# Kernel optimization log

Measured on AMD Instinct MI355X. Metric: run time of the kernel, lower is better.

The kernel has to match this reference:

```python
import jax, jax.numpy as jnp
import numpy as np

BETA, ALPHA, NS_STEPS = 0.9, 1.0, 1
D_MODEL, D_STATE, D_CONV, EXPAND = 768, 16, 4, 2
D_INNER = EXPAND * D_MODEL
DT_RANK = -(-D_MODEL // 16)  # ceil(d_model/16) = 48
B, L = 2, 1024


def setup_inputs() -> dict:
    key = jax.random.key(0)
    ks = jax.random.split(key, 8)
    s = lambda k, shape, sc=0.02: jax.random.normal(k, shape, jnp.float32) * sc
    return {
        "hidden_states": jax.random.normal(ks[0], (B, L, D_MODEL), jnp.float32),
        "in_proj_w": s(ks[1], (2 * D_INNER, D_MODEL)),
        "conv_w": s(ks[2], (D_INNER, 1, D_CONV), 0.2),
        "conv_b": jnp.zeros((D_INNER,), jnp.float32),
        "x_proj_w": s(ks[3], (DT_RANK + 2 * D_STATE, D_INNER)),
        "dt_head_w": s(ks[4], (D_INNER, DT_RANK)),
        "dt_head_b": s(ks[5], (D_INNER,), 0.1),
        "out_proj_w": s(ks[6], (D_MODEL, D_INNER)),
        "D": jnp.ones((D_INNER,), jnp.float32),
    }


def _newton_schulz(G, steps):
    """Muon-style quintic Newton-Schulz orthogonalization of (b, d, n) with d >= n."""
    a, b, c = 3.4445, -4.7750, 2.0315
    X = G / (jnp.linalg.norm(G, axis=(-2, -1), keepdims=True) + 1e-7)
    X = X.swapaxes(-2, -1)  # (b, n, d): rows <= cols
    for _ in range(steps):
        A = X @ X.swapaxes(-2, -1)       # (b, n, n) small Gram
        Bm = b * A + c * (A @ A)
        X = a * X + Bm @ X
    return X.swapaxes(-2, -1)            # back to (b, d, n)


def reference(hidden_states, in_proj_w, conv_w, conv_b, x_proj_w, dt_head_w, dt_head_b, out_proj_w, D):
    Bz, Lz, _ = hidden_states.shape
    dtype = hidden_states.dtype
    # input projection -> x, z  (B, L, d_inner) each
    xz = jnp.einsum('bld,ed->ble', hidden_states, in_proj_w)
    x, z = jnp.split(xz, 2, axis=-1)
    # causal depthwise conv over time + SiLU
    xc = jax.lax.conv_general_dilated(
        x.swapaxes(1, 2), conv_w, (1,), [(D_CONV - 1, 0)],
        dimension_numbers=('NCH', 'OIH', 'NCH'), feature_group_count=D_INNER)
    x = jax.nn.silu(xc.swapaxes(1, 2) + conv_b)  # (B, L, d_inner)
    # projections for dt / k / q
    x_dbl = jnp.einsum('bld,ed->ble', x, x_proj_w)
    dt_low, k, q = jnp.split(x_dbl, [DT_RANK, DT_RANK + D_STATE], axis=-1)
    dt = jnp.einsum('blr,dr->bld', dt_low, dt_head_w)  # (B, L, d_inner), bias applied in scan

    def step(carry, inp):
        v, h = carry  # velocity / hidden states, each (b, d_inner, d_state)
        x_t, dt_t, k_t, q_t = inp
        dt_t = jax.nn.sigmoid(dt_t + dt_head_b)                              # (b, d)
        dt_t = dt_t / (1.0 + dt_t * jnp.sum(k_t * k_t, axis=-1, keepdims=True))
        dA = 1.0 - dt_t[:, :, None] * (k_t * k_t)[:, None, :]                # (b, d, n)
        G = (dt_t * x_t)[:, :, None] * k_t[:, None, :]                       # dt * u * k
        v = BETA * v + ALPHA * _newton_schulz(G, NS_STEPS)
        h = dA * h + v
        y_t = jnp.einsum('bdn,bn->bd', h, q_t) + D * x_t
        return (v, h), y_t

    init = (jnp.zeros((Bz, D_INNER, D_STATE), dtype),
            jnp.zeros((Bz, D_INNER, D_STATE), dtype))
    xs = (x.swapaxes(0, 1), dt.swapaxes(0, 1), k.swapaxes(0, 1), q.swapaxes(0, 1))
    _, y = jax.lax.scan(step, init, xs)        # (L, B, d_inner)
    y = y.swapaxes(0, 1) * jax.nn.silu(z)      # gate
    return jnp.einsum('bld,od->blo', y, out_proj_w)
```

## Files before the change

kernel.cpp:

```cpp
#include <hip/hip_runtime.h>

#define D_MODEL 768
#define D_STATE 16
#define D_INNER 1536
#define DT_RANK 48
#define NB 2
#define LSEQ 1024
#define NROWS (NB * LSEQ)
#define CCH 8
#define CLEN (LSEQ / CCH)
#define BETA_CL 1.3900845e-06f

typedef __attribute__((ext_vector_type(4))) float f32x4;
typedef __attribute__((ext_vector_type(8))) short s16x8;
typedef __attribute__((ext_vector_type(8))) unsigned short u16x8;

__device__ __forceinline__ unsigned short f2bu(float f) {
  unsigned int x = __builtin_bit_cast(unsigned int, f);
  x += 0x7fffu + ((x >> 16) & 1u);
  return (unsigned short)(x >> 16);
}

typedef __attribute__((address_space(3))) unsigned int as3u32;
typedef __attribute__((address_space(1))) const unsigned int as1u32;
__device__ __forceinline__ void gload16(const unsigned short* g, unsigned short* l) {
  __builtin_amdgcn_global_load_lds((as1u32*)g, (as3u32*)l, 16, 0, 0);
}

#define CVT_TOTAL 663552
#define Z1_GROUPS 20480
#define Z2_GROUPS 196608
__global__ __launch_bounds__(256) void cvt5z_kernel(const float* __restrict__ s0,
                                                    const float* __restrict__ s1,
                                                    const float* __restrict__ s2,
                                                    const float* __restrict__ s3,
                                                    const float* __restrict__ s4,
                                                    unsigned short* __restrict__ d0,
                                                    unsigned short* __restrict__ d1,
                                                    unsigned short* __restrict__ d2,
                                                    unsigned short* __restrict__ d3,
                                                    unsigned short* __restrict__ d4,
                                                    float* __restrict__ z1,
                                                    float* __restrict__ z2) {
  int g = blockIdx.x * 256 + threadIdx.x;
  if (g >= CVT_TOTAL) {
    int zg = g - CVT_TOTAL;
    f32x4 zero = {0.f, 0.f, 0.f, 0.f};
    if (zg < Z1_GROUPS) {
      *(f32x4*)(z1 + zg * 8) = zero;
      *(f32x4*)(z1 + zg * 8 + 4) = zero;
    } else if (zg < Z1_GROUPS + Z2_GROUPS) {
      int i = (zg - Z1_GROUPS) * 8;
      *(f32x4*)(z2 + i) = zero;
      *(f32x4*)(z2 + i + 4) = zero;
    }
    return;
  }
  const float* s;
  unsigned short* d;
  int base;
  if (g < 196608)      { s = s0; d = d0; base = 0; }
  else if (g < 491520) { s = s1; d = d1; base = 196608; }
  else if (g < 506880) { s = s2; d = d2; base = 491520; }
  else if (g < 516096) { s = s3; d = d3; base = 506880; }
  else                 { s = s4; d = d4; base = 516096; }
  int i = (g - base) * 8;
  f32x4 a = *(const f32x4*)(s + i);
  f32x4 b = *(const f32x4*)(s + i + 4);
  u16x8 o;
#pragma unroll
  for (int j = 0; j < 4; j++) { o[j] = f2bu(a[j]); o[4 + j] = f2bu(b[j]); }
  *(u16x8*)(d + i) = o;
}

template <bool ATOMIC>
__global__ __launch_bounds__(256) void gemm128(const unsigned short* __restrict__ A,
                                               const unsigned short* __restrict__ B,
                                               float* __restrict__ C, int K,
                                               int lda, int ldb, int ldc, int kseg_len) {
  __shared__ __align__(16) unsigned short As[2][128 * 32];
  __shared__ __align__(16) unsigned short Bs[2][128 * 32];
  const int m0 = blockIdx.y * 128, n0 = blockIdx.x * 128;
  const int kbeg = blockIdx.z * kseg_len;
  const int kend = kbeg + kseg_len;
  const int t = threadIdx.x;
  const int wave = t >> 6, lane = t & 63;
  const int wm = wave >> 1, wn = wave & 1;
  const int quad = lane >> 4, l16 = lane & 15;
  const int srow = lane >> 2;
  const int kcol = (lane & 3) * 8;

  auto stage = [&](int bi, int k0) {
#pragma unroll
    for (int r = 0; r < 2; r++) {
      const int seg = r * 64 + wave * 16;
      gload16(A + (size_t)(m0 + seg + srow) * lda + k0 + kcol, &As[bi][seg * 32]);
      gload16(B + (size_t)(n0 + seg + srow) * ldb + k0 + kcol, &Bs[bi][seg * 32]);
    }
  };

  f32x4 acc[4][4] = {};
  stage(0, kbeg);
  __syncthreads();
  int buf = 0;
  for (int k0 = kbeg; k0 < kend; k0 += 32) {
    if (k0 + 32 < kend) stage(buf ^ 1, k0 + 32);
    s16x8 af[4], bf[4];
#pragma unroll
    for (int i = 0; i < 4; i++) {
      af[i] = *(const s16x8*)&As[buf][(wm * 64 + i * 16 + l16) * 32 + quad * 8];
      bf[i] = *(const s16x8*)&Bs[buf][(wn * 64 + i * 16 + l16) * 32 + quad * 8];
    }
#pragma unroll
    for (int mi = 0; mi < 4; mi++)
#pragma unroll
      for (int ni = 0; ni < 4; ni++)
        acc[mi][ni] = __builtin_amdgcn_mfma_f32_16x16x32_bf16(af[mi], bf[ni], acc[mi][ni], 0, 0, 0);
    __syncthreads();
    buf ^= 1;
  }
#pragma unroll
  for (int mi = 0; mi < 4; mi++)
#pragma unroll
    for (int ni = 0; ni < 4; ni++)
#pragma unroll
      for (int r = 0; r < 4; r++) {
        int row = m0 + wm * 64 + mi * 16 + quad * 4 + r;
        int col = n0 + wn * 64 + ni * 16 + l16;
        if constexpr (ATOMIC)
          atomicAdd(&C[(size_t)row * ldc + col], acc[mi][ni][r]);
        else
          C[(size_t)row * ldc + col] = acc[mi][ni][r];
      }
}

template <bool AF32, bool ATOMIC>
__global__ __launch_bounds__(256) void gemm_bt(const void* __restrict__ Av,
                                               const unsigned short* __restrict__ B,
                                               float* __restrict__ C, int M, int N, int K,
                                               int lda, int ldb, int ldc, int kseg_len) {
  __shared__ __align__(16) unsigned short As[2][64][40];
  __shared__ __align__(16) unsigned short Bs[2][64][40];
  const int m0 = blockIdx.y * 64, n0 = blockIdx.x * 64;
  const int kbeg = blockIdx.z * kseg_len;
  const int kend = (kbeg + kseg_len < K) ? (kbeg + kseg_len) : K;
  const int t = threadIdx.x;
  const int wave = t >> 6, lane = t & 63;
  const int wm = wave >> 1, wn = wave & 1;
  const int quad = lane >> 4, l16 = lane & 15;
  const int srow = t >> 2;
  const int kseg = (t & 3) * 8;
  const bool va = (m0 + srow) < M, vb = (n0 + srow) < N;
  const float* Af = (const float*)Av;
  const unsigned short* Ab = (const unsigned short*)Av;
  const unsigned short* Bp = B + (size_t)(n0 + srow) * ldb;

  f32x4 ra0, ra1;
  u16x8 rab, rbb;
  auto pref = [&](int k0) {
    const int kk = k0 + kseg;
    const int krem = kend - kk;
    if constexpr (AF32) {
      const float* Ap = Af + (size_t)(m0 + srow) * lda + kk;
      if (va && krem >= 8) {
        ra0 = *(const f32x4*)Ap;
        ra1 = *(const f32x4*)(Ap + 4);
      } else {
#pragma unroll
        for (int j = 0; j < 4; j++) {
          ra0[j] = (va && j < krem) ? Ap[j] : 0.0f;
          ra1[j] = (va && j + 4 < krem) ? Ap[j + 4] : 0.0f;
        }
      }
    } else {
      const unsigned short* Ap = Ab + (size_t)(m0 + srow) * lda + kk;
      if (va && krem >= 8) {
        rab = *(const u16x8*)Ap;
      } else {
#pragma unroll
        for (int j = 0; j < 8; j++) rab[j] = (va && j < krem) ? Ap[j] : (unsigned short)0;
      }
    }
    if (vb && krem >= 8) {
      rbb = *(const u16x8*)(Bp + kk);
    } else {
#pragma unroll
      for (int j = 0; j < 8; j++) rbb[j] = (vb && j < krem) ? Bp[kk + j] : (unsigned short)0;
    }
  };
  auto tolds = [&](int bi) {
    if constexpr (AF32) {
      u16x8 oa;
#pragma unroll
      for (int j = 0; j < 4; j++) { oa[j] = f2bu(ra0[j]); oa[4 + j] = f2bu(ra1[j]); }
      *(u16x8*)&As[bi][srow][kseg] = oa;
    } else {
      *(u16x8*)&As[bi][srow][kseg] = rab;
    }
    *(u16x8*)&Bs[bi][srow][kseg] = rbb;
  };

  f32x4 acc[2][2] = {};
  pref(kbeg);
  tolds(0);
  __syncthreads();
  int buf = 0;
  for (int k0 = kbeg; k0 < kend; k0 += 32) {
    const bool more = (k0 + 32 < kend);
    if (more) pref(k0 + 32);
    s16x8 a0 = *(const s16x8*)&As[buf][wm * 32 + l16][quad * 8];
    s16x8 a1 = *(const s16x8*)&As[buf][wm * 32 + 16 + l16][quad * 8];
    s16x8 b0 = *(const s16x8*)&Bs[buf][wn * 32 + l16][quad * 8];
    s16x8 b1 = *(const s16x8*)&Bs[buf][wn * 32 + 16 + l16][quad * 8];
    acc[0][0] = __builtin_amdgcn_mfma_f32_16x16x32_bf16(a0, b0, acc[0][0], 0, 0, 0);
    acc[0][1] = __builtin_amdgcn_mfma_f32_16x16x32_bf16(a0, b1, acc[0][1], 0, 0, 0);
    acc[1][0] = __builtin_amdgcn_mfma_f32_16x16x32_bf16(a1, b0, acc[1][0], 0, 0, 0);
    acc[1][1] = __builtin_amdgcn_mfma_f32_16x16x32_bf16(a1, b1, acc[1][1], 0, 0, 0);
    if (more) tolds(buf ^ 1);
    __syncthreads();
    buf ^= 1;
  }
#pragma unroll
  for (int mi = 0; mi < 2; mi++)
#pragma unroll
    for (int ni = 0; ni < 2; ni++)
#pragma unroll
      for (int r = 0; r < 4; r++) {
        int row = m0 + wm * 32 + mi * 16 + quad * 4 + r;
        int col = n0 + wn * 32 + ni * 16 + l16;
        if (row < M && col < N) {
          if constexpr (ATOMIC)
            atomicAdd(&C[(size_t)row * ldc + col], acc[mi][ni][r]);
          else
            C[(size_t)row * ldc + col] = acc[mi][ni][r];
        }
      }
}

__global__ __launch_bounds__(256) void conv_silu_kernel(const float* __restrict__ xz,
                                                        const float* __restrict__ cw,
                                                        const float* __restrict__ cb,
                                                        float* __restrict__ xc,
                                                        unsigned short* __restrict__ xcb) {
  int idx = blockIdx.x * 256 + threadIdx.x;
  if (idx >= NROWS * D_INNER) return;
  int c = idx % D_INNER;
  int row = idx / D_INNER;
  int l = row & (LSEQ - 1);
  float acc = cb[c];
#pragma unroll
  for (int j = 0; j < 4; j++) {
    int dl = l - 3 + j;
    if (dl >= 0) acc += xz[(size_t)(row - 3 + j) * 3072 + c] * cw[c * 4 + j];
  }
  float sg = 1.0f / (1.0f + expf(-acc));
  float val = acc * sg;
  xc[idx] = val;
  xcb[idx] = f2bu(val);
}

__global__ __launch_bounds__(256) void precompute_kernel(const float* __restrict__ xdbl,
                                                         float* __restrict__ dtbuf,
                                                         const float* __restrict__ xconv,
                                                         const float* __restrict__ dtb,
                                                         float* __restrict__ ubuf,
                                                         float* __restrict__ kqbuf) {
  int row = blockIdx.x;
  int t = threadIdx.x;
  const float* xr = xdbl + (size_t)row * 80;
  float nk = 0.0f;
#pragma unroll
  for (int n = 0; n < 16; n++) { float kv = xr[48 + n]; nk += kv * kv; }
  float dtf[6], u0[6];
  float nupart = 0.0f;
#pragma unroll
  for (int i = 0; i < 6; i++) {
    int d = i * 256 + t;
    float draw = dtbuf[(size_t)row * D_INNER + d] + dtb[d];
    float sg = 1.0f / (1.0f + expf(-draw));
    float dv = sg / (1.0f + sg * nk);
    dtf[i] = dv;
    float u = dv * xconv[(size_t)row * D_INNER + d];
    u0[i] = u;
    nupart += u * u;
  }
  __shared__ float red[4];
  float v = nupart;
#pragma unroll
  for (int off = 32; off > 0; off >>= 1) v += __shfl_xor(v, off);
  if ((t & 63) == 0) red[t >> 6] = v;
  __syncthreads();
  float nu = red[0] + red[1] + red[2] + red[3];
  float p = nu * nk;
  float s = sqrtf(p) + 1e-7f;
  float tt = p / (s * s);
  float gamma = (3.4445f + tt * (-4.7750f + 2.0315f * tt)) / s;
#pragma unroll
  for (int i = 0; i < 6; i++) {
    int d = i * 256 + t;
    dtbuf[(size_t)row * D_INNER + d] = dtf[i];
    ubuf[(size_t)row * D_INNER + d] = gamma * u0[i];
  }
  if (t < 16) {
    kqbuf[(size_t)row * 32 + t] = xr[48 + t];
    kqbuf[(size_t)row * 32 + 16 + t] = xr[64 + t];
  }
}

__global__ __launch_bounds__(64) void scan_phase1(const float* __restrict__ ubuf,
                                                  const float* __restrict__ dtbuf,
                                                  const float* __restrict__ kqbuf,
                                                  float* __restrict__ cvp,
                                                  float* __restrict__ chp,
                                                  float* __restrict__ gp,
                                                  float* __restrict__ rp) {
  __shared__ float u_s[2][32][16];
  __shared__ float dt_s[2][32][16];
  __shared__ __align__(16) float kq_s[2][32][32];
  const int t = threadIdx.x;
  const int nq = t & 3, dloc = t >> 2;
  const int b = blockIdx.x / (96 * CCH);
  const int rem = blockIdx.x % (96 * CCH);
  const int d0 = (rem / CCH) * 16;
  const int c = rem % CCH;
  const int tbase = c * CLEN;
  const size_t ub = (size_t)b * LSEQ * D_INNER + d0;
  const float* kqb = kqbuf + (size_t)b * LSEQ * 32;
  const int scol = t & 15, srow0 = t >> 4;
  const int krow0 = t >> 3, kcol = (t & 7) * 4;
  float pu[8], pd[8];
  f32x4 pk[4];
  auto prefetch = [&](int t0) {
#pragma unroll
    for (int i = 0; i < 8; i++) {
      size_t off = ub + (size_t)(t0 + srow0 + 4 * i) * D_INNER + scol;
      pu[i] = ubuf[off];
      pd[i] = dtbuf[off];
    }
#pragma unroll
    for (int i = 0; i < 4; i++)
      pk[i] = *(const f32x4*)(kqb + (size_t)(t0 + krow0 + 8 * i) * 32 + kcol);
  };
  auto writelds = [&](int bi) {
#pragma unroll
    for (int i = 0; i < 8; i++) {
      u_s[bi][srow0 + 4 * i][scol] = pu[i];
      dt_s[bi][srow0 + 4 * i][scol] = pd[i];
    }
#pragma unroll
    for (int i = 0; i < 4; i++)
      *(f32x4*)&kq_s[bi][krow0 + 8 * i][kcol] = pk[i];
  };
  f32x4 v = {0.f, 0.f, 0.f, 0.f}, h = {0.f, 0.f, 0.f, 0.f};
  f32x4 g = {0.f, 0.f, 0.f, 0.f}, r = {1.f, 1.f, 1.f, 1.f};
  float bt = 0.9f;
  prefetch(tbase);
  writelds(0);
  int buf = 0;
  for (int t0 = 0; t0 < CLEN; t0 += 32) {
    const bool more = (t0 + 32 < CLEN);
    if (more) prefetch(tbase + t0 + 32);
#pragma unroll 4
    for (int s = 0; s < 32; s++) {
      float u = u_s[buf][s][dloc];
      float dtf = dt_s[buf][s][dloc];
      f32x4 kv = *(const f32x4*)&kq_s[buf][s][nq * 4];
#pragma unroll
      for (int j = 0; j < 4; j++) {
        float kj = kv[j];
        v[j] = fmaf(0.9f, v[j], u * kj);
        float a = fmaf(-dtf * kj, kj, 1.0f);
        h[j] = fmaf(a, h[j], v[j]);
        r[j] *= a;
        g[j] = fmaf(a, g[j], bt);
      }
      bt *= 0.9f;
    }
    if (more) writelds(buf ^ 1);
    buf ^= 1;
  }
  size_t o = (((size_t)b * CCH + c) * D_INNER + d0 + dloc) * 16 + nq * 4;
  *(f32x4*)(cvp + o) = v;
  *(f32x4*)(chp + o) = h;
  *(f32x4*)(gp + o) = g;
  *(f32x4*)(rp + o) = r;
}

__global__ __launch_bounds__(256) void scan_phase2(const float* __restrict__ cvp,
                                                   const float* __restrict__ chp,
                                                   float* __restrict__ gp,
                                                   float* __restrict__ rp) {
  int i = blockIdx.x * 256 + threadIdx.x;
  int b = i / (D_INNER * 16);
  int rem = i % (D_INNER * 16);
  float v0 = 0.f, h0 = 0.f;
#pragma unroll
  for (int c = 0; c < CCH; c++) {
    size_t o = ((size_t)(b * CCH + c)) * (D_INNER * 16) + rem;
    float cv = cvp[o], ch = chp[o], gg = gp[o], rr = rp[o];
    gp[o] = v0;
    rp[o] = h0;
    float v0n = fmaf(BETA_CL, v0, cv);
    float h0n = fmaf(gg, v0, fmaf(rr, h0, ch));
    v0 = v0n;
    h0 = h0n;
  }
}

__global__ __launch_bounds__(64) void scan_phase3(const float* __restrict__ ubuf,
                                                  const float* __restrict__ dtbuf,
                                                  const float* __restrict__ kqbuf,
                                                  const float* __restrict__ gp,
                                                  const float* __restrict__ rp,
                                                  const float* __restrict__ xconv,
                                                  const float* __restrict__ xz,
                                                  const float* __restrict__ Dp,
                                                  unsigned short* __restrict__ ygb) {
  __shared__ float u_s[2][32][16];
  __shared__ float dt_s[2][32][16];
  __shared__ __align__(16) float kq_s[2][32][32];
  __shared__ float xc_s[2][32][16];
  __shared__ float z_s[2][32][16];
  const int t = threadIdx.x;
  const int nq = t & 3, dloc = t >> 2;
  const int b = blockIdx.x / (96 * CCH);
  const int rem = blockIdx.x % (96 * CCH);
  const int d0 = (rem / CCH) * 16;
  const int c = rem % CCH;
  const int tbase = c * CLEN;
  const size_t ub = (size_t)b * LSEQ * D_INNER + d0;
  const float* kqb = kqbuf + (size_t)b * LSEQ * 32;
  const float* xzb = xz + (size_t)b * LSEQ * 3072 + 1536 + d0;
  unsigned short* y_p = ygb + (size_t)b * LSEQ * D_INNER + d0 + dloc;
  const int scol = t & 15, srow0 = t >> 4;
  const int krow0 = t >> 3, kcol = (t & 7) * 4;
  float pu[8], pd[8], pxc[8], pz[8];
  f32x4 pk[4];
  auto prefetch = [&](int t0) {
#pragma unroll
    for (int i = 0; i < 8; i++) {
      size_t off = ub + (size_t)(t0 + srow0 + 4 * i) * D_INNER + scol;
      pu[i] = ubuf[off];
      pd[i] = dtbuf[off];
      pxc[i] = xconv[off];
      pz[i] = xzb[(size_t)(t0 + srow0 + 4 * i) * 3072 + scol];
    }
#pragma unroll
    for (int i = 0; i < 4; i++)
      pk[i] = *(const f32x4*)(kqb + (size_t)(t0 + krow0 + 8 * i) * 32 + kcol);
  };
  auto writelds = [&](int bi) {
#pragma unroll
    for (int i = 0; i < 8; i++) {
      u_s[bi][srow0 + 4 * i][scol] = pu[i];
      dt_s[bi][srow0 + 4 * i][scol] = pd[i];
      xc_s[bi][srow0 + 4 * i][scol] = pxc[i];
      z_s[bi][srow0 + 4 * i][scol] = pz[i];
    }
#pragma unroll
    for (int i = 0; i < 4; i++)
      *(f32x4*)&kq_s[bi][krow0 + 8 * i][kcol] = pk[i];
  };
  size_t so = (((size_t)b * CCH + c) * D_INNER + d0 + dloc) * 16 + nq * 4;
  f32x4 v = *(const f32x4*)(gp + so);
  f32x4 h = *(const f32x4*)(rp + so);
  const float Dd = Dp[d0 + dloc];
  prefetch(tbase);
  writelds(0);
  int buf = 0;
  for (int t0 = 0; t0 < CLEN; t0 += 32) {
    const bool more = (t0 + 32 < CLEN);
    if (more) prefetch(tbase + t0 + 32);
#pragma unroll 4
    for (int s = 0; s < 32; s++) {
      float u = u_s[buf][s][dloc];
      float dtf = dt_s[buf][s][dloc];
      f32x4 kv = *(const f32x4*)&kq_s[buf][s][nq * 4];
      f32x4 qv = *(const f32x4*)&kq_s[buf][s][16 + nq * 4];
      float yp = 0.0f;
#pragma unroll
      for (int j = 0; j < 4; j++) {
        float kj = kv[j];
        v[j] = fmaf(0.9f, v[j], u * kj);
        float dA = fmaf(-dtf * kj, kj, 1.0f);
        h[j] = fmaf(dA, h[j], v[j]);
        yp = fmaf(h[j], qv[j], yp);
      }
      yp += __shfl_xor(yp, 1);
      yp += __shfl_xor(yp, 2);
      float zv = z_s[buf][s][dloc];
      float sz = zv / (1.0f + expf(-zv));
      float val = (yp + Dd * xc_s[buf][s][dloc]) * sz;
      if (nq == 0) y_p[(size_t)(tbase + t0 + s) * D_INNER] = f2bu(val);
    }
    if (more) writelds(buf ^ 1);
    buf ^= 1;
  }
}

extern "C" void kernel_launch(void* const* d_in, const int* in_sizes, int n_in,
                              void* d_out, int out_size, void* d_ws, size_t ws_size,
                              hipStream_t stream) {
  const float* hidden = (const float*)d_in[0];
  const float* w_in   = (const float*)d_in[1];
  const float* conv_w = (const float*)d_in[2];
  const float* conv_b = (const float*)d_in[3];
  const float* w_x    = (const float*)d_in[4];
  const float* w_dt   = (const float*)d_in[5];
  const float* b_dt   = (const float*)d_in[6];
  const float* w_out  = (const float*)d_in[7];
  const float* Dp     = (const float*)d_in[8];

  float* ws    = (float*)d_ws;
  float* xz    = ws;
  float* xconv = xz + (size_t)NROWS * 3072;
  float* xdbl  = xconv + (size_t)NROWS * D_INNER;
  float* dtbuf = xdbl + (size_t)NROWS * 80;
  float* ubuf  = dtbuf + (size_t)NROWS * D_INNER;
  float* kqbuf = ubuf + (size_t)NROWS * D_INNER;
  float* ybuf  = kqbuf + (size_t)NROWS * 32;
  const size_t PL = (size_t)NB * CCH * D_INNER * 16;
  float* cvp   = ybuf + (size_t)NROWS * D_INNER;
  float* chp   = cvp + PL;
  float* gp    = chp + PL;
  float* rp    = gp + PL;
  unsigned short* bfr = (unsigned short*)(rp + PL);
  unsigned short* hbf = bfr;
  unsigned short* wib = hbf + 1572864;
  unsigned short* wxb = wib + 2359296;
  unsigned short* wdb = wxb + 122880;
  unsigned short* wob = wdb + 73728;
  unsigned short* xcb = wob + 1179648;
  unsigned short* ygb = xcb + 3145728;

  dim3 blk(256);
  cvt5z_kernel<<<dim3((CVT_TOTAL + Z1_GROUPS + Z2_GROUPS) / 256), blk, 0, stream>>>(
      hidden, w_in, w_x, w_dt, w_out, hbf, wib, wxb, wdb, wob, xdbl, (float*)d_out);
  gemm128<false><<<dim3(24, 16, 1), blk, 0, stream>>>(hbf, wib, xz, 768, 768, 768, 3072, 768);
  conv_silu_kernel<<<dim3(12288), blk, 0, stream>>>(xz, conv_w, conv_b, xconv, xcb);
  gemm_bt<false, true><<<dim3(2, 32, 8), blk, 0, stream>>>(xcb, wxb, xdbl, 2048, 80, 1536,
                                                           1536, 1536, 80, 192);
  gemm_bt<true, false><<<dim3(24, 32, 1), blk, 0, stream>>>(xdbl, wdb, dtbuf, 2048, 1536, 48,
                                                            80, 48, 1536, 48);
  precompute_kernel<<<dim3(NROWS), blk, 0, stream>>>(xdbl, dtbuf, xconv, b_dt, ubuf, kqbuf);
  scan_phase1<<<dim3(NB * 96 * CCH), dim3(64), 0, stream>>>(ubuf, dtbuf, kqbuf, cvp, chp, gp, rp);
  scan_phase2<<<dim3(192), blk, 0, stream>>>(cvp, chp, gp, rp);
  scan_phase3<<<dim3(NB * 96 * CCH), dim3(64), 0, stream>>>(ubuf, dtbuf, kqbuf, gp, rp,
                                                            xconv, xz, Dp, ygb);
  gemm128<true><<<dim3(6, 16, 4), blk, 0, stream>>>(ygb, wob, (float*)d_out, 1536,
                                                    1536, 1536, 768, 384);
}
```

Before: 229.7 us.

## Split scan into more time chunks and use wider 256-thread blocks

The chunked linear scan now uses 16 time chunks instead of 8, which halves each block's serial recurrence length. The chunk-carry decay constant is updated to 0.9^64 to match. The phase-1 and phase-3 scan kernels now run 256-thread blocks covering 64 channels, staging 16 timesteps at a time in LDS, with added __syncthreads barriers since multiple waves share the tiles. The unused ybuf workspace region is dropped to make room for the doubled chunk-partial buffers. The trade-off is more phase-2 combine work and barrier overhead per staging step.

```diff
diff --git a/kernel.cpp b/kernel.cpp
--- a/kernel.cpp
+++ b/kernel.cpp
@@ -7,9 +7,10 @@
 #define NB 2
 #define LSEQ 1024
 #define NROWS (NB * LSEQ)
-#define CCH 8
+#define CCH 16
 #define CLEN (LSEQ / CCH)
-#define BETA_CL 1.3900845e-06f
+#define STP 16
+#define BETA_CL 1.1790185e-03f
 
 typedef __attribute__((ext_vector_type(4))) float f32x4;
 typedef __attribute__((ext_vector_type(8))) short s16x8;
@@ -307,61 +308,58 @@
   }
 }
 
-__global__ __launch_bounds__(64) void scan_phase1(const float* __restrict__ ubuf,
-                                                  const float* __restrict__ dtbuf,
-                                                  const float* __restrict__ kqbuf,
-                                                  float* __restrict__ cvp,
-                                                  float* __restrict__ chp,
-                                                  float* __restrict__ gp,
-                                                  float* __restrict__ rp) {
-  __shared__ float u_s[2][32][16];
-  __shared__ float dt_s[2][32][16];
-  __shared__ __align__(16) float kq_s[2][32][32];
+__global__ __launch_bounds__(256) void scan_phase1(const float* __restrict__ ubuf,
+                                                   const float* __restrict__ dtbuf,
+                                                   const float* __restrict__ kqbuf,
+                                                   float* __restrict__ cvp,
+                                                   float* __restrict__ chp,
+                                                   float* __restrict__ gp,
+                                                   float* __restrict__ rp) {
+  __shared__ float u_s[2][STP][64];
+  __shared__ float dt_s[2][STP][64];
+  __shared__ __align__(16) float kq_s[2][STP][36];
   const int t = threadIdx.x;
   const int nq = t & 3, dloc = t >> 2;
-  const int b = blockIdx.x / (96 * CCH);
-  const int rem = blockIdx.x % (96 * CCH);
-  const int d0 = (rem / CCH) * 16;
+  const int b = blockIdx.x / (24 * CCH);
+  const int rem = blockIdx.x % (24 * CCH);
+  const int d0 = (rem / CCH) * 64;
   const int c = rem % CCH;
   const int tbase = c * CLEN;
   const size_t ub = (size_t)b * LSEQ * D_INNER + d0;
   const float* kqb = kqbuf + (size_t)b * LSEQ * 32;
-  const int scol = t & 15, srow0 = t >> 4;
-  const int krow0 = t >> 3, kcol = (t & 7) * 4;
-  float pu[8], pd[8];
-  f32x4 pk[4];
+  const int scol = t & 63, srow0 = t >> 6;
+  const int krow = t >> 3, kcol = (t & 7) * 4;
+  float pu[4], pd[4];
+  f32x4 pk;
   auto prefetch = [&](int t0) {
 #pragma unroll
-    for (int i = 0; i < 8; i++) {
+    for (int i = 0; i < 4; i++) {
       size_t off = ub + (size_t)(t0 + srow0 + 4 * i) * D_INNER + scol;
       pu[i] = ubuf[off];
       pd[i] = dtbuf[off];
     }
-#pragma unroll
-    for (int i = 0; i < 4; i++)
-      pk[i] = *(const f32x4*)(kqb + (size_t)(t0 + krow0 + 8 * i) * 32 + kcol);
+    if (t < 128) pk = *(const f32x4*)(kqb + (size_t)(t0 + krow) * 32 + kcol);
   };
   auto writelds = [&](int bi) {
 #pragma unroll
-    for (int i = 0; i < 8; i++) {
+    for (int i = 0; i < 4; i++) {
       u_s[bi][srow0 + 4 * i][scol] = pu[i];
       dt_s[bi][srow0 + 4 * i][scol] = pd[i];
     }
-#pragma unroll
-    for (int i = 0; i < 4; i++)
-      *(f32x4*)&kq_s[bi][krow0 + 8 * i][kcol] = pk[i];
+    if (t < 128) *(f32x4*)&kq_s[bi][krow][kcol] = pk;
   };
   f32x4 v = {0.f, 0.f, 0.f, 0.f}, h = {0.f, 0.f, 0.f, 0.f};
   f32x4 g = {0.f, 0.f, 0.f, 0.f}, r = {1.f, 1.f, 1.f, 1.f};
   float bt = 0.9f;
   prefetch(tbase);
   writelds(0);
+  __syncthreads();
   int buf = 0;
-  for (int t0 = 0; t0 < CLEN; t0 += 32) {
-    const bool more = (t0 + 32 < CLEN);
-    if (more) prefetch(tbase + t0 + 32);
+  for (int t0 = 0; t0 < CLEN; t0 += STP) {
+    const bool more = (t0 + STP < CLEN);
+    if (more) prefetch(tbase + t0 + STP);
 #pragma unroll 4
-    for (int s = 0; s < 32; s++) {
+    for (int s = 0; s < STP; s++) {
       float u = u_s[buf][s][dloc];
       float dtf = dt_s[buf][s][dloc];
       f32x4 kv = *(const f32x4*)&kq_s[buf][s][nq * 4];
@@ -377,6 +375,7 @@
       bt *= 0.9f;
     }
     if (more) writelds(buf ^ 1);
+    __syncthreads();
     buf ^= 1;
   }
   size_t o = (((size_t)b * CCH + c) * D_INNER + d0 + dloc) * 16 + nq * 4;
@@ -407,59 +406,55 @@
   }
 }
 
-__global__ __launch_bounds__(64) void scan_phase3(const float* __restrict__ ubuf,
-                                                  const float* __restrict__ dtbuf,
-                                                  const float* __restrict__ kqbuf,
-                                                  const float* __restrict__ gp,
-                                                  const float* __restrict__ rp,
-                                                  const float* __restrict__ xconv,
-                                                  const float* __restrict__ xz,
-                                                  const float* __restrict__ Dp,
-                                                  unsigned short* __restrict__ ygb) {
-  __shared__ float u_s[2][32][16];
-  __shared__ float dt_s[2][32][16];
-  __shared__ __align__(16) float kq_s[2][32][32];
-  __shared__ float xc_s[2][32][16];
-  __shared__ float z_s[2][32][16];
+__global__ __launch_bounds__(256) void scan_phase3(const float* __restrict__ ubuf,
+                                                   const float* __restrict__ dtbuf,
+                                                   const float* __restrict__ kqbuf,
+                                                   const float* __restrict__ gp,
+                                                   const float* __restrict__ rp,
+                                                   const float* __restrict__ xconv,
+                                                   const float* __restrict__ xz,
+                                                   const float* __restrict__ Dp,
+                                                   unsigned short* __restrict__ ygb) {
+  __shared__ float u_s[2][STP][64];
+  __shared__ float dt_s[2][STP][64];
+  __shared__ float xc_s[2][STP][64];
+  __shared__ float z_s[2][STP][64];
+  __shared__ __align__(16) float kq_s[2][STP][36];
   const int t = threadIdx.x;
   const int nq = t & 3, dloc = t >> 2;
-  const int b = blockIdx.x / (96 * CCH);
-  const int rem = blockIdx.x % (96 * CCH);
-  const int d0 = (rem / CCH) * 16;
+  const int b = blockIdx.x / (24 * CCH);
+  const int rem = blockIdx.x % (24 * CCH);
+  const int d0 = (rem / CCH) * 64;
   const int c = rem % CCH;
   const int tbase = c * CLEN;
   const size_t ub = (size_t)b * LSEQ * D_INNER + d0;
   const float* kqb = kqbuf + (size_t)b * LSEQ * 32;
   const float* xzb = xz + (size_t)b * LSEQ * 3072 + 1536 + d0;
   unsigned short* y_p = ygb + (size_t)b * LSEQ * D_INNER + d0 + dloc;
-  const int scol = t & 15, srow0 = t >> 4;
-  const int krow0 = t >> 3, kcol = (t & 7) * 4;
-  float pu[8], pd[8], pxc[8], pz[8];
-  f32x4 pk[4];
+  const int scol = t & 63, srow0 = t >> 6;
+  const int krow = t >> 3, kcol = (t & 7) * 4;
+  float pu[4], pd[4], pxc[4], pz[4];
+  f32x4 pk;
   auto prefetch = [&](int t0) {
 #pragma unroll
-    for (int i = 0; i < 8; i++) {
+    for (int i = 0; i < 4; i++) {
       size_t off = ub + (size_t)(t0 + srow0 + 4 * i) * D_INNER + scol;
       pu[i] = ubuf[off];
       pd[i] = dtbuf[off];
       pxc[i] = xconv[off];
       pz[i] = xzb[(size_t)(t0 + srow0 + 4 * i) * 3072 + scol];
     }
-#pragma unroll
-    for (int i = 0; i < 4; i++)
-      pk[i] = *(const f32x4*)(kqb + (size_t)(t0 + krow0 + 8 * i) * 32 + kcol);
+    if (t < 128) pk = *(const f32x4*)(kqb + (size_t)(t0 + krow) * 32 + kcol);
   };
   auto writelds = [&](int bi) {
 #pragma unroll
-    for (int i = 0; i < 8; i++) {
+    for (int i = 0; i < 4; i++) {
       u_s[bi][srow0 + 4 * i][scol] = pu[i];
       dt_s[bi][srow0 + 4 * i][scol] = pd[i];
       xc_s[bi][srow0 + 4 * i][scol] = pxc[i];
       z_s[bi][srow0 + 4 * i][scol] = pz[i];
     }
-#pragma unroll
-    for (int i = 0; i < 4; i++)
-      *(f32x4*)&kq_s[bi][krow0 + 8 * i][kcol] = pk[i];
+    if (t < 128) *(f32x4*)&kq_s[bi][krow][kcol] = pk;
   };
   size_t so = (((size_t)b * CCH + c) * D_INNER + d0 + dloc) * 16 + nq * 4;
   f32x4 v = *(const f32x4*)(gp + so);
@@ -467,12 +462,13 @@
   const float Dd = Dp[d0 + dloc];
   prefetch(tbase);
   writelds(0);
+  __syncthreads();
   int buf = 0;
-  for (int t0 = 0; t0 < CLEN; t0 += 32) {
-    const bool more = (t0 + 32 < CLEN);
-    if (more) prefetch(tbase + t0 + 32);
+  for (int t0 = 0; t0 < CLEN; t0 += STP) {
+    const bool more = (t0 + STP < CLEN);
+    if (more) prefetch(tbase + t0 + STP);
 #pragma unroll 4
-    for (int s = 0; s < 32; s++) {
+    for (int s = 0; s < STP; s++) {
       float u = u_s[buf][s][dloc];
       float dtf = dt_s[buf][s][dloc];
       f32x4 kv = *(const f32x4*)&kq_s[buf][s][nq * 4];
@@ -494,6 +490,7 @@
       if (nq == 0) y_p[(size_t)(tbase + t0 + s) * D_INNER] = f2bu(val);
     }
     if (more) writelds(buf ^ 1);
+    __syncthreads();
     buf ^= 1;
   }
 }
@@ -518,9 +515,8 @@
   float* dtbuf = xdbl + (size_t)NROWS * 80;
   float* ubuf  = dtbuf + (size_t)NROWS * D_INNER;
   float* kqbuf = ubuf + (size_t)NROWS * D_INNER;
-  float* ybuf  = kqbuf + (size_t)NROWS * 32;
   const size_t PL = (size_t)NB * CCH * D_INNER * 16;
-  float* cvp   = ybuf + (size_t)NROWS * D_INNER;
+  float* cvp   = kqbuf + (size_t)NROWS * 32;
   float* chp   = cvp + PL;
   float* gp    = chp + PL;
   float* rp    = gp + PL;
@@ -543,10 +539,10 @@
   gemm_bt<true, false><<<dim3(24, 32, 1), blk, 0, stream>>>(xdbl, wdb, dtbuf, 2048, 1536, 48,
                                                             80, 48, 1536, 48);
   precompute_kernel<<<dim3(NROWS), blk, 0, stream>>>(xdbl, dtbuf, xconv, b_dt, ubuf, kqbuf);
-  scan_phase1<<<dim3(NB * 96 * CCH), dim3(64), 0, stream>>>(ubuf, dtbuf, kqbuf, cvp, chp, gp, rp);
+  scan_phase1<<<dim3(NB * 24 * CCH), blk, 0, stream>>>(ubuf, dtbuf, kqbuf, cvp, chp, gp, rp);
   scan_phase2<<<dim3(192), blk, 0, stream>>>(cvp, chp, gp, rp);
-  scan_phase3<<<dim3(NB * 96 * CCH), dim3(64), 0, stream>>>(ubuf, dtbuf, kqbuf, gp, rp,
-                                                            xconv, xz, Dp, ygb);
+  scan_phase3<<<dim3(NB * 24 * CCH), blk, 0, stream>>>(ubuf, dtbuf, kqbuf, gp, rp,
+                                                       xconv, xz, Dp, ygb);
   gemm128<true><<<dim3(6, 16, 4), blk, 0, stream>>>(ygb, wob, (float*)d_out, 1536,
                                                     1536, 1536, 768, 384);
 }
```

Result: faster. 215.6 us (-6.2%).
